# Kernel optimization log

Measured on AMD Instinct MI355X. Metric: run time of the kernel, lower is better.

The kernel has to match this reference:

```python
import jax, jax.numpy as jnp
import numpy as np

BN_EPS = 1e-5

def setup_inputs() -> dict:
    key = jax.random.key(0)
    k1, k2 = jax.random.split(key)
    B, C, H, W, K = 256, 2048, 7, 7, 16
    featmap = jax.random.normal(k1, (B, C, H, W), dtype=jnp.float32)
    w16 = jax.random.normal(k2, (K, C), dtype=jnp.float32) * 0.02  # 1x1 conv weight
    bn_gamma = jnp.ones((K,), jnp.float32)
    bn_beta = jnp.zeros((K,), jnp.float32)
    bn_mean = jnp.zeros((K,), jnp.float32)
    bn_var = jnp.ones((K,), jnp.float32)
    return {"featmap": featmap, "w16": w16, "bn_gamma": bn_gamma,
            "bn_beta": bn_beta, "bn_mean": bn_mean, "bn_var": bn_var}

def reference(featmap, w16, bn_gamma, bn_beta, bn_mean, bn_var):
    # featmap: [B, 2048, 7, 7]; 1x1 conv -> featcov16: [B, 16, 7, 7]
    featcov16 = jnp.einsum('bchw,kc->bkhw', featmap, w16)
    # BatchNorm2d(16), inference-style with running stats
    inv = bn_gamma / jnp.sqrt(bn_var + BN_EPS)
    featcov16 = featcov16 * inv[None, :, None, None] + (bn_beta - bn_mean * inv)[None, :, None, None]
    # Loop-free bilinear pooling: original repeats featcov16[:,i] to 2048 ch,
    # multiplies with featmap, and AvgPool2d(7) -> mean over HxW.
    HW = featmap.shape[2] * featmap.shape[3]
    feat_matrix = jnp.einsum('bkhw,bchw->bkc', featcov16, featmap) / HW  # [B,16,2048]
    bp_out_feat = feat_matrix.reshape(feat_matrix.shape[0], -1)  # [B, 32768]
    return bp_out_feat
```

## Files before the change

kernel.cpp:

```cpp
#include <hip/hip_runtime.h>

#define BATCH 256
#define CDIM  2048
#define HW    49
#define KDIM  16

__global__ __launch_bounds__(256) void pconv_kernel(
    const float* __restrict__ fm, const float* __restrict__ w16,
    float* __restrict__ Ppart)
{
    __shared__ __align__(16) float red[4 * 784];

    const int tid  = threadIdx.x;
    const int lane = tid & 63;
    const int wv   = __builtin_amdgcn_readfirstlane(tid >> 6);
    const int b    = blockIdx.x >> 2;
    const int q    = blockIdx.x & 3;

    float acc[16];
    #pragma unroll
    for (int k = 0; k < 16; ++k) acc[k] = 0.f;

    if (lane < HW) {
        const float* fmb = fm + (size_t)b * CDIM * HW + lane;
        const int cbase = q * 512 + wv * 128;
        #pragma unroll 2
        for (int c4 = 0; c4 < 128; c4 += 4) {
            const int cg = cbase + c4;
            float f0 = fmb[(cg + 0) * HW];
            float f1 = fmb[(cg + 1) * HW];
            float f2 = fmb[(cg + 2) * HW];
            float f3 = fmb[(cg + 3) * HW];
            #pragma unroll
            for (int k = 0; k < 16; ++k) {
                const float4 wq = *(const float4*)(w16 + k * CDIM + cg);
                acc[k] += wq.x * f0 + wq.y * f1 + wq.z * f2 + wq.w * f3;
            }
        }
    }

    if (lane < HW) {
        #pragma unroll
        for (int k4 = 0; k4 < 4; ++k4) {
            float4 v;
            v.x = acc[k4 * 4 + 0]; v.y = acc[k4 * 4 + 1];
            v.z = acc[k4 * 4 + 2]; v.w = acc[k4 * 4 + 3];
            *(float4*)&red[wv * 784 + lane * 16 + k4 * 4] = v;
        }
    }
    __syncthreads();
    if (tid < 196) {
        const int e = tid * 4;
        float4 a0 = *(const float4*)&red[e];
        float4 a1 = *(const float4*)&red[784 + e];
        float4 a2 = *(const float4*)&red[1568 + e];
        float4 a3 = *(const float4*)&red[2352 + e];
        float4 o;
        o.x = a0.x + a1.x + a2.x + a3.x;
        o.y = a0.y + a1.y + a2.y + a3.y;
        o.z = a0.z + a1.z + a2.z + a3.z;
        o.w = a0.w + a1.w + a2.w + a3.w;
        *(float4*)(Ppart + (size_t)blockIdx.x * 784 + e) = o;
    }
}

__global__ __launch_bounds__(256) void preduce_kernel(
    const float* __restrict__ Ppart,
    const float* __restrict__ gamma, const float* __restrict__ beta,
    const float* __restrict__ mean, const float* __restrict__ var,
    float* __restrict__ Pbn)
{
    const int b = blockIdx.x;
    const float* pp = Ppart + (size_t)b * 4 * 784;
    for (int p = threadIdx.x; p < 784; p += 256) {
        float s = pp[p] + pp[p + 784] + pp[p + 1568] + pp[p + 2352];
        const int kk = p & 15;
        float inv   = gamma[kk] * rsqrtf(var[kk] + 1e-5f);
        float shift = beta[kk] - mean[kk] * inv;
        Pbn[(size_t)b * 784 + p] = (s * inv + shift) * (1.0f / 49.0f);
    }
}

__global__ __launch_bounds__(256) void bp_kernel(
    const float* __restrict__ fm, const float* __restrict__ Pbn,
    float* __restrict__ out)
{
    __shared__ __align__(16) float fm_s[256 * HW];

    const int tid = threadIdx.x;
    const int b   = blockIdx.x >> 3;
    const int c0  = (blockIdx.x & 7) * 256;

    const float4* src = (const float4*)(fm + ((size_t)b * CDIM + c0) * HW);
    float4* dst = (float4*)fm_s;
    #pragma unroll
    for (int i = 0; i < 12; ++i) dst[i * 256 + tid] = src[i * 256 + tid];
    if (tid < 64) dst[3072 + tid] = src[3072 + tid];
    __syncthreads();

    float f[HW];
    #pragma unroll
    for (int i = 0; i < HW; ++i) f[i] = fm_s[tid * HW + i];

    const float* Pb = Pbn + (size_t)b * 784;

    float acc[16];
    #pragma unroll
    for (int i = 0; i < 16; ++i) acc[i] = 0.f;

    #pragma unroll
    for (int hw = 0; hw < HW; ++hw) {
        const float4 p0 = *(const float4*)(Pb + hw * 16 + 0);
        const float4 p1 = *(const float4*)(Pb + hw * 16 + 4);
        const float4 p2 = *(const float4*)(Pb + hw * 16 + 8);
        const float4 p3 = *(const float4*)(Pb + hw * 16 + 12);
        const float fv = f[hw];
        acc[0]  += p0.x * fv; acc[1]  += p0.y * fv; acc[2]  += p0.z * fv; acc[3]  += p0.w * fv;
        acc[4]  += p1.x * fv; acc[5]  += p1.y * fv; acc[6]  += p1.z * fv; acc[7]  += p1.w * fv;
        acc[8]  += p2.x * fv; acc[9]  += p2.y * fv; acc[10] += p2.z * fv; acc[11] += p2.w * fv;
        acc[12] += p3.x * fv; acc[13] += p3.y * fv; acc[14] += p3.z * fv; acc[15] += p3.w * fv;
    }

    float* ob = out + (size_t)b * (KDIM * CDIM) + c0 + tid;
    #pragma unroll
    for (int kk = 0; kk < 16; ++kk) ob[kk * CDIM] = acc[kk];
}

extern "C" void kernel_launch(void* const* d_in, const int* in_sizes, int n_in,
                              void* d_out, int out_size, void* d_ws, size_t ws_size,
                              hipStream_t stream) {
    const float* fm    = (const float*)d_in[0];
    const float* w16   = (const float*)d_in[1];
    const float* gamma = (const float*)d_in[2];
    const float* beta  = (const float*)d_in[3];
    const float* mean  = (const float*)d_in[4];
    const float* var   = (const float*)d_in[5];
    float* out   = (float*)d_out;
    float* Ppart = (float*)d_ws;
    float* Pbn   = Ppart + (size_t)1024 * 784;

    pconv_kernel<<<BATCH * 4, 256, 0, stream>>>(fm, w16, Ppart);
    preduce_kernel<<<BATCH, 256, 0, stream>>>(Ppart, gamma, beta, mean, var, Pbn);
    bp_kernel<<<BATCH * 8, 256, 0, stream>>>(fm, Pbn, out);
}
```

Before: 227.8 us.

## Broadcast weights and pooled projections via readlane instead of redundant global loads

In pconv, each wave now loads a 16x64 slice of the weight matrix once into per-lane registers. It then broadcasts each scalar with readlane, instead of every lane issuing the same float4 weight loads for each channel. In bp_kernel, the 784 BN'd projection values are loaded into 13 registers per lane and broadcast with readlane. This replaces the per-thread uniform global loads of Pbn and the 49-register row copy from LDS. The aim is to cut redundant memory and cache traffic, at the cost of many readlane (SALU/VALU) instructions that may serialize.

```diff
diff --git a/kernel.cpp b/kernel.cpp
--- a/kernel.cpp
+++ b/kernel.cpp
@@ -4,6 +4,10 @@
 #define CDIM  2048
 #define HW    49
 #define KDIM  16
+
+__device__ __forceinline__ float rl(float v, int l) {
+    return __int_as_float(__builtin_amdgcn_readlane(__float_as_int(v), l));
+}
 
 __global__ __launch_bounds__(256) void pconv_kernel(
     const float* __restrict__ fm, const float* __restrict__ w16,
@@ -16,25 +20,40 @@
     const int wv   = __builtin_amdgcn_readfirstlane(tid >> 6);
     const int b    = blockIdx.x >> 2;
     const int q    = blockIdx.x & 3;
+    const int cbase = q * 512 + wv * 128;
+
+    const int kw = lane & 15;
+    const int sw = lane >> 4;
+    const int lrow = (lane < HW) ? lane : (HW - 1);
+    const float* fmb = fm + (size_t)b * CDIM * HW + lrow;
 
     float acc[16];
     #pragma unroll
     for (int k = 0; k < 16; ++k) acc[k] = 0.f;
 
-    if (lane < HW) {
-        const float* fmb = fm + (size_t)b * CDIM * HW + lane;
-        const int cbase = q * 512 + wv * 128;
-        #pragma unroll 2
-        for (int c4 = 0; c4 < 128; c4 += 4) {
-            const int cg = cbase + c4;
-            float f0 = fmb[(cg + 0) * HW];
-            float f1 = fmb[(cg + 1) * HW];
-            float f2 = fmb[(cg + 2) * HW];
-            float f3 = fmb[(cg + 3) * HW];
+    #pragma unroll 1
+    for (int j2 = 0; j2 < 2; ++j2) {
+        const int cg0 = cbase + j2 * 64;
+        float wreg[16];
+        {
+            const float* wp = w16 + kw * CDIM + cg0 + sw;
+            #pragma unroll
+            for (int jj = 0; jj < 16; ++jj) wreg[jj] = wp[jj * 4];
+        }
+        const float* fmc = fmb + (size_t)cg0 * HW;
+        #pragma unroll
+        for (int jj = 0; jj < 16; ++jj) {
+            float f0 = fmc[(jj * 4 + 0) * HW];
+            float f1 = fmc[(jj * 4 + 1) * HW];
+            float f2 = fmc[(jj * 4 + 2) * HW];
+            float f3 = fmc[(jj * 4 + 3) * HW];
+            const float wsrc = wreg[jj];
             #pragma unroll
             for (int k = 0; k < 16; ++k) {
-                const float4 wq = *(const float4*)(w16 + k * CDIM + cg);
-                acc[k] += wq.x * f0 + wq.y * f1 + wq.z * f2 + wq.w * f3;
+                acc[k] += rl(wsrc, k)      * f0
+                        + rl(wsrc, 16 + k) * f1
+                        + rl(wsrc, 32 + k) * f2
+                        + rl(wsrc, 48 + k) * f3;
             }
         }
     }
@@ -87,9 +106,16 @@
 {
     __shared__ __align__(16) float fm_s[256 * HW];
 
-    const int tid = threadIdx.x;
-    const int b   = blockIdx.x >> 3;
-    const int c0  = (blockIdx.x & 7) * 256;
+    const int tid  = threadIdx.x;
+    const int lane = tid & 63;
+    const int b    = blockIdx.x >> 3;
+    const int c0   = (blockIdx.x & 7) * 256;
+
+    const float* Pb = Pbn + (size_t)b * 784;
+    float preg[13];
+    #pragma unroll
+    for (int j = 0; j < 12; ++j) preg[j] = Pb[j * 64 + lane];
+    preg[12] = Pb[768 + (lane & 15)];
 
     const float4* src = (const float4*)(fm + ((size_t)b * CDIM + c0) * HW);
     float4* dst = (float4*)fm_s;
@@ -98,27 +124,19 @@
     if (tid < 64) dst[3072 + tid] = src[3072 + tid];
     __syncthreads();
 
-    float f[HW];
-    #pragma unroll
-    for (int i = 0; i < HW; ++i) f[i] = fm_s[tid * HW + i];
-
-    const float* Pb = Pbn + (size_t)b * 784;
-
     float acc[16];
     #pragma unroll
     for (int i = 0; i < 16; ++i) acc[i] = 0.f;
 
+    const float* row = fm_s + tid * HW;
     #pragma unroll
     for (int hw = 0; hw < HW; ++hw) {
-        const float4 p0 = *(const float4*)(Pb + hw * 16 + 0);
-        const float4 p1 = *(const float4*)(Pb + hw * 16 + 4);
-        const float4 p2 = *(const float4*)(Pb + hw * 16 + 8);
-        const float4 p3 = *(const float4*)(Pb + hw * 16 + 12);
-        const float fv = f[hw];
-        acc[0]  += p0.x * fv; acc[1]  += p0.y * fv; acc[2]  += p0.z * fv; acc[3]  += p0.w * fv;
-        acc[4]  += p1.x * fv; acc[5]  += p1.y * fv; acc[6]  += p1.z * fv; acc[7]  += p1.w * fv;
-        acc[8]  += p2.x * fv; acc[9]  += p2.y * fv; acc[10] += p2.z * fv; acc[11] += p2.w * fv;
-        acc[12] += p3.x * fv; acc[13] += p3.y * fv; acc[14] += p3.z * fv; acc[15] += p3.w * fv;
+        const float f = row[hw];
+        #pragma unroll
+        for (int k = 0; k < 16; ++k) {
+            const int p = hw * 16 + k;
+            acc[k] += rl(preg[p >> 6], p & 63) * f;
+        }
     }
 
     float* ob = out + (size_t)b * (KDIM * CDIM) + c0 + tid;
```

Result: faster. 219.0 us (-3.9%).
